# Kernel optimization log

Hardware: AMD Instinct MI355X
Metric: run time of the kernel (lower is better)

## Reference

```python
import jax, jax.numpy as jnp
import numpy as np

B, TQ, TK, D, R, H = 4, 2048, 2048, 1024, 64, 512
TAU_BASE, ASTRO_DECAY = 1.0, 0.95


def setup_inputs() -> dict:
    key = jax.random.key(0)
    ks = jax.random.split(key, 20)
    xav = lambda k, din, dout: jax.random.uniform(k, (din, dout), jnp.float32, -1.0, 1.0) * np.sqrt(6.0 / (din + dout))
    inp = {
        'q_in': jax.random.normal(ks[0], (B, TQ, D), jnp.float32),
        'k_in': jax.random.normal(ks[1], (B, TK, D), jnp.float32),
        'v_in': jax.random.normal(ks[2], (B, TK, D), jnp.float32),
        'astrocyte_state': jnp.zeros((B,), jnp.float32),
        'Wq': xav(ks[3], D, D), 'bq': jnp.zeros((D,), jnp.float32),
        'Wk': xav(ks[4], D, D), 'bk': jnp.zeros((D,), jnp.float32),
        'Wv': xav(ks[5], D, D), 'bv': jnp.zeros((D,), jnp.float32),
        'Wo': xav(ks[6], D, D), 'bo': jnp.zeros((D,), jnp.float32),
        # orthonormal role rows (R <= D): QR of a random D x R matrix, rows = Q^T
        'role_matrix': jnp.linalg.qr(jax.random.normal(ks[7], (D, R), jnp.float32))[0].T,
        'Wr1': xav(ks[8], D, H), 'br1': jnp.zeros((H,), jnp.float32),
        'Wr2': xav(ks[9], H, R),
        'astro_scale': jnp.ones((1,), jnp.float32),
    }
    return inp


def _l2norm(x, axis=-1, eps=1e-12):
    return x / jnp.clip(jnp.linalg.norm(x, axis=axis, keepdims=True), eps)


def _bind_vectors(a, b):
    # holographic (circular-convolution) binding via FFT along feature dim
    n = a.shape[-1]
    return jnp.fft.irfft(jnp.fft.rfft(a, axis=-1) * jnp.fft.rfft(b, axis=-1), n=n, axis=-1)


def _compute_surprise(Q):
    # per-token surprise: RMS-normalized L2 magnitude of projected queries -> (B, T_q)
    return jnp.linalg.norm(Q, axis=-1) / np.sqrt(Q.shape[-1])


def reference(q_in, k_in, v_in, astrocyte_state, Wq, bq, Wk, bk, Wv, bv, Wo, bo,
              role_matrix, Wr1, br1, Wr2, astro_scale):
    Q = q_in @ Wq + bq                      # (B,TQ,D)
    K = k_in @ Wk + bk                      # (B,TK,D)
    V = v_in @ Wv + bv                      # (B,TK,D)

    role_mat_norm = _l2norm(role_matrix)    # (R,D)
    role_logits = jax.nn.relu(K @ Wr1 + br1) @ Wr2          # (B,TK,R)
    role_weights = jax.nn.softmax(role_logits, axis=-1)
    role_vecs = role_weights @ role_mat_norm                 # (B,TK,D)
    K_bound = _bind_vectors(K, role_vecs)                    # (B,TK,D)

    surprise = _compute_surprise(Q)                          # (B,TQ)
    mean_surprise = surprise.mean(axis=-1)                   # (B,)
    new_state = ASTRO_DECAY * astrocyte_state + (1.0 - ASTRO_DECAY) * mean_surprise
    tau_eff = TAU_BASE * jnp.clip(1.0 + astro_scale * new_state, 0.001)[:, None, None]

    q_n = _l2norm(Q)
    k_n = _l2norm(K_bound)
    cos_sim = jnp.einsum('bqd,bkd->bqk', q_n, k_n)           # (B,TQ,TK)
    x = (cos_sim + 1.0) * 0.5
    scores = jnp.clip(1.0 - tau_eff * (1.0 - x) ** 2, 0.0)   # Epanechnikov kernel
    attn = scores / jnp.clip(scores.sum(axis=-1, keepdims=True), 1e-9)
    context = jnp.einsum('bqk,bkd->bqd', attn, V)
    output = context @ Wo + bo
    return output, new_state
```

## Files before the change

kernel.cpp:

```cpp
#include <hip/hip_runtime.h>
#include <stdint.h>


#define Bq 4
#define Tq 2048
#define Dd 1024
#define NT 8192
#define Hh 512
#define Rr_ 64
#define FP 640
#define F2 1280

typedef unsigned short ushort_t;
typedef short s16x8 __attribute__((ext_vector_type(8)));
typedef float floatx4 __attribute__((ext_vector_type(4)));

__device__ __forceinline__ float b2f(ushort_t s) {
  unsigned u = (unsigned)s << 16;
  return __builtin_bit_cast(float, u);
}
__device__ __forceinline__ ushort_t f2b(float f) {
  unsigned u = __builtin_bit_cast(unsigned, f);
  unsigned r = (u + 0x7fffu + ((u >> 16) & 1u)) >> 16;
  return (ushort_t)r;
}

__device__ __forceinline__ void load_lds16(const void* g, void* l) {
  __builtin_amdgcn_global_load_lds((__attribute__((address_space(1))) void*)(g),
                                   (__attribute__((address_space(3))) void*)(l),
                                   16, 0, 0);
}

__global__ __launch_bounds__(256) void gemm_bt(
    const ushort_t* __restrict__ A, const ushort_t* __restrict__ Bt,
    float* __restrict__ C, ushort_t* __restrict__ Cbf,
    const float* __restrict__ bias, const float* __restrict__ tau,
    float* __restrict__ rowsum, int rsStride, int rsMode,
    int K, int lda, int ldb, int ldc,
    long long sA, long long sB, long long sC, int flags)
{
  __shared__ __align__(16) ushort_t As[128 * 32];
  __shared__ __align__(16) ushort_t Bs[128 * 32];

  const int bz   = blockIdx.z;
  const ushort_t* Ab = A + (size_t)bz * sA;
  const ushort_t* Bb = Bt + (size_t)bz * sB;
  const int tm   = blockIdx.y * 128;
  const int tn   = blockIdx.x * 128;
  const int tid  = threadIdx.x;
  const int wave = tid >> 6;
  const int lane = tid & 63;
  const int wm   = (wave & 1) << 6;
  const int wn   = (wave >> 1) << 6;
  const int sr   = lane >> 2;
  const int sc   = (lane & 3) << 3;
  const int fr   = lane & 15;
  const int fk   = (lane >> 4) << 3;

  floatx4 acc[4][4] = {};

  for (int k0 = 0; k0 < K; k0 += 32) {
    {
      const ushort_t* gA0 = Ab + (size_t)(tm + wave * 16 + sr) * lda + (k0 + sc);
      const ushort_t* gA1 = gA0 + (size_t)64 * lda;
      char* lA = (char*)As + wave * 1024;
      load_lds16(gA0, lA);
      load_lds16(gA1, lA + 4096);
      const ushort_t* gB0 = Bb + (size_t)(tn + wave * 16 + sr) * ldb + (k0 + sc);
      const ushort_t* gB1 = gB0 + (size_t)64 * ldb;
      char* lB = (char*)Bs + wave * 1024;
      load_lds16(gB0, lB);
      load_lds16(gB1, lB + 4096);
    }
    __syncthreads();
    s16x8 af[4], bfv[4];
#pragma unroll
    for (int i = 0; i < 4; i++)
      af[i] = *(const s16x8*)&As[(wm + i * 16 + fr) * 32 + fk];
#pragma unroll
    for (int j = 0; j < 4; j++)
      bfv[j] = *(const s16x8*)&Bs[(wn + j * 16 + fr) * 32 + fk];
#pragma unroll
    for (int i = 0; i < 4; i++)
#pragma unroll
      for (int j = 0; j < 4; j++)
        acc[i][j] = __builtin_amdgcn_mfma_f32_16x16x32_bf16(af[i], bfv[j], acc[i][j], 0, 0, 0);
    __syncthreads();
  }

  const float tv = tau ? tau[bz] : 0.f;
  float*   Cp  = C   ? C   + (size_t)bz * sC : nullptr;
  ushort_t* Cb = Cbf ? Cbf + (size_t)bz * sC : nullptr;
#pragma unroll
  for (int i = 0; i < 4; i++) {
#pragma unroll
    for (int r = 0; r < 4; r++) {
      const int row = tm + wm + i * 16 + (lane >> 4) * 4 + r;
      float rsum = 0.f;
      float dinv = 1.f;
      if (rsMode == 3)
        dinv = 1.f / fmaxf(rowsum[(size_t)bz * rsStride + row], 1e-9f);
#pragma unroll
      for (int j = 0; j < 4; j++) {
        const int col = tn + wn + j * 16 + (lane & 15);
        float v = acc[i][j][r];
        if (bias) v += bias[col];
        if (flags & 1) v = fmaxf(v, 0.f);
        if (tau) { float d = 1.0f - v; v = fmaxf(1.0f - tv * 0.25f * d * d, 0.f); }
        if (rsMode == 3) v *= dinv;
        rsum += (rsMode == 2) ? v * v : v;
        if (Cp) Cp[(size_t)row * ldc + col] = v;
        if (Cb) Cb[(size_t)row * ldc + col] = f2b(v);
      }
      if (rsMode == 1 || rsMode == 2) {
        rsum += __shfl_xor(rsum, 1);
        rsum += __shfl_xor(rsum, 2);
        rsum += __shfl_xor(rsum, 4);
        rsum += __shfl_xor(rsum, 8);
        if ((lane & 15) == 0)
          atomicAdd(&rowsum[(size_t)bz * rsStride + row], rsum);
      }
    }
  }
}

__global__ __launch_bounds__(256) void castbf(const float* __restrict__ in,
                                              ushort_t* __restrict__ out, int n4) {
  int i = blockIdx.x * 256 + threadIdx.x;
  if (i >= n4) return;
  float4 v = ((const float4*)in)[i];
  ushort4 o;
  o.x = f2b(v.x); o.y = f2b(v.y); o.z = f2b(v.z); o.w = f2b(v.w);
  ((ushort4*)out)[i] = o;
}

__global__ __launch_bounds__(256) void tcast(const float* __restrict__ in,
                                             ushort_t* __restrict__ out,
                                             int RrN, int Cc, int Cp) {
  __shared__ float t[32][33];
  int r0 = blockIdx.x * 32, c0 = blockIdx.y * 32;
  int x = threadIdx.x, y = threadIdx.y;
  for (int dy = 0; dy < 32; dy += 8) {
    int r = r0 + y + dy, c = c0 + x;
    t[y + dy][x] = (c < Cc) ? in[(size_t)r * Cc + c] : 0.f;
  }
  __syncthreads();
  for (int dy = 0; dy < 32; dy += 8) {
    int c = c0 + y + dy, r = r0 + x;
    if (c < Cp) out[(size_t)c * RrN + r] = f2b(t[x][y + dy]);
  }
}

__global__ __launch_bounds__(512) void transpose_bf(const ushort_t* __restrict__ in,
                                                    ushort_t* __restrict__ out,
                                                    int RrN, int Cc, long long sIn, long long sOut) {
  __shared__ ushort_t t[64][65];
  int z = blockIdx.z;
  int r0 = blockIdx.y * 64, c0 = blockIdx.x * 64;
  int x = threadIdx.x, y = threadIdx.y;
  const ushort_t* ip = in + (size_t)z * sIn;
  ushort_t* op = out + (size_t)z * sOut;
  for (int dy = 0; dy < 64; dy += 8)
    t[y + dy][x] = ip[(size_t)(r0 + y + dy) * Cc + c0 + x];
  __syncthreads();
  for (int dy = 0; dy < 64; dy += 8)
    op[(size_t)(c0 + y + dy) * RrN + r0 + x] = t[x][y + dy];
}

__global__ __launch_bounds__(256) void rolenorm(const float* __restrict__ rm,
                                                ushort_t* __restrict__ rmn) {
  int r = blockIdx.x, tid = threadIdx.x;
  float4 v = ((const float4*)(rm + (size_t)r * 1024))[tid];
  float s = v.x * v.x + v.y * v.y + v.z * v.z + v.w * v.w;
#pragma unroll
  for (int m = 1; m < 64; m <<= 1) s += __shfl_xor(s, m);
  __shared__ float red[6];
  if ((tid & 63) == 0) red[tid >> 6] = s;
  __syncthreads();
  if (tid == 0) red[4] = 1.f / fmaxf(sqrtf(red[0] + red[1] + red[2] + red[3]), 1e-12f);
  __syncthreads();
  float inv = red[4];
  ushort4 o;
  o.x = f2b(v.x * inv); o.y = f2b(v.y * inv); o.z = f2b(v.z * inv); o.w = f2b(v.w * inv);
  ((ushort4*)(rmn + (size_t)r * 1024))[tid] = o;
}

__global__ __launch_bounds__(256) void rfn_kernel(const ushort_t* __restrict__ rmn,
                                                  const ushort_t* __restrict__ ftab,
                                                  ushort_t* __restrict__ RFnT) {
  int f = blockIdx.x;
  int t = threadIdx.x;
  int r = t >> 2, part = t & 3;
  const ushort_t* fr = ftab + (size_t)f * 1024 + part * 256;
  const ushort_t* rr = rmn + (size_t)r * 1024 + part * 256;
  float s = 0.f;
#pragma unroll 4
  for (int i = 0; i < 32; i++) {
    s16x8 a = *(const s16x8*)(fr + i * 8);
    s16x8 b = *(const s16x8*)(rr + i * 8);
#pragma unroll
    for (int j = 0; j < 8; j++) s += b2f((ushort_t)a[j]) * b2f((ushort_t)b[j]);
  }
  s += __shfl_xor(s, 1);
  s += __shfl_xor(s, 2);
  if (part == 0) RFnT[(size_t)f * 128 + r] = f2b(s);
}

__global__ __launch_bounds__(256) void scale_rows(const ushort_t* __restrict__ in,
                                                  ushort_t* __restrict__ out,
                                                  const float* __restrict__ sumsq) {
  int gid = blockIdx.x * 256 + threadIdx.x;
  int row = gid >> 7;
  int c0 = (gid & 127) << 3;
  float inv = 1.f / fmaxf(sqrtf(sumsq[row]), 1e-12f);
  const s16x8* p = (const s16x8*)(in + (size_t)row * 1024 + c0);
  s16x8 v = *p;
  s16x8 o;
#pragma unroll
  for (int i = 0; i < 8; i++) o[i] = (short)f2b(b2f((ushort_t)v[i]) * inv);
  *(s16x8*)(out + (size_t)row * 1024 + c0) = o;
}

__global__ __launch_bounds__(256) void surprise_sum(const float* __restrict__ sumsq,
                                                    float* __restrict__ ssum) {
  int row = blockIdx.x * 256 + threadIdx.x;
  float nrm = sqrtf(sumsq[row]);
#pragma unroll
  for (int m = 1; m < 64; m <<= 1) nrm += __shfl_xor(nrm, m);
  if ((threadIdx.x & 63) == 0) atomicAdd(&ssum[row >> 11], nrm);
}

__global__ void finalize_astro(const float* __restrict__ ssum, const float* __restrict__ astro,
                               const float* __restrict__ ascale, float* __restrict__ tau,
                               float* __restrict__ outTail) {
  int b = threadIdx.x;
  if (b < Bq) {
    float mean = ssum[b] * (1.f / (32.f * 2048.f));
    float ns = 0.95f * astro[b] + 0.05f * mean;
    tau[b] = fmaxf(1.f + ascale[0] * ns, 0.001f);
    outTail[b] = ns;
  }
}

__global__ __launch_bounds__(256) void softmax64(const float* __restrict__ logits,
                                                 ushort_t* __restrict__ out) {
  int row = blockIdx.x * 4 + (threadIdx.x >> 6);
  int lane = threadIdx.x & 63;
  float x = logits[(size_t)row * 128 + lane];
  float m = x;
#pragma unroll
  for (int s = 1; s < 64; s <<= 1) m = fmaxf(m, __shfl_xor(m, s));
  float e = expf(x - m);
  float sum = e;
#pragma unroll
  for (int s = 1; s < 64; s <<= 1) sum += __shfl_xor(sum, s);
  out[(size_t)row * 64 + lane] = f2b(e / sum);
}

__global__ __launch_bounds__(256) void gen_ftab(ushort_t* __restrict__ ftab) {
  const float TW = 6.283185307179586f / 1024.f;
  int idx = blockIdx.x * 256 + threadIdx.x;
  int rowf = idx >> 10, k = idx & 1023;
  int f = rowf < FP ? rowf : rowf - FP;
  float v = 0.f;
  if (f <= 512) {
    float th = (float)((f * k) & 1023) * TW;
    float sv, cv; sincosf(th, &sv, &cv);
    v = (rowf < FP) ? cv : -sv;
  }
  ftab[idx] = f2b(v);
}
__global__ __launch_bounds__(256) void gen_itab(ushort_t* __restrict__ itab) {
  const float TW = 6.283185307179586f / 1024.f;
  int idx = blockIdx.x * 256 + threadIdx.x;
  int n = idx / F2;
  int c = idx - n * F2;
  int f = c < FP ? c : c - FP;
  float v = 0.f;
  if (f <= 512) {
    float w = (f == 0 || f == 512) ? (1.f / 1024.f) : (2.f / 1024.f);
    float th = (float)((f * n) & 1023) * TW;
    float sv, cv; sincosf(th, &sv, &cv);
    v = (c < FP) ? w * cv : -w * sv;
  }
  itab[idx] = f2b(v);
}

__global__ __launch_bounds__(256) void fftmul(const ushort_t* __restrict__ KF,
                                              const ushort_t* __restrict__ RF,
                                              ushort_t* __restrict__ P) {
  int idx = blockIdx.x * 256 + threadIdx.x;
  int t = idx / FP;
  int f = idx - t * FP;
  size_t base = (size_t)t * F2;
  float a = b2f(KF[base + f]), b = b2f(KF[base + FP + f]);
  float c = b2f(RF[base + f]), d = b2f(RF[base + FP + f]);
  P[base + f]      = f2b(a * c - b * d);
  P[base + FP + f] = f2b(a * d + b * c);
}

static constexpr size_t OFF_RS    = 0;
static constexpr size_t OFF_SSQQ  = 32768;
static constexpr size_t OFF_SSQK  = 65536;
static constexpr size_t OFF_SSUM  = 98304;
static constexpr size_t OFF_TAU   = 98320;
static constexpr size_t OFF_WQT   = 98816;
static constexpr size_t OFF_WKT   = OFF_WQT  + 2097152;
static constexpr size_t OFF_WVT   = OFF_WKT  + 2097152;
static constexpr size_t OFF_WOT   = OFF_WVT  + 2097152;
static constexpr size_t OFF_WR1T  = OFF_WOT  + 2097152;
static constexpr size_t OFF_WR2T  = OFF_WR1T + 1048576;
static constexpr size_t OFF_RMN   = OFF_WR2T + 131072;
static constexpr size_t OFF_FTAB  = OFF_RMN  + 131072;
static constexpr size_t OFF_ITAB  = OFF_FTAB + 2621440;
static constexpr size_t OFF_RFNT  = OFF_ITAB + 2621440;
static constexpr size_t OFF_R1    = OFF_RFNT + 327680;
static constexpr size_t OFF_R2    = OFF_R1   + 20971520;
static constexpr size_t OFF_R3    = OFF_R2   + 20971520;
static constexpr size_t OFF_R4    = OFF_R3   + 20971520;
static constexpr size_t OFF_R5    = OFF_R4   + 16777216;
static constexpr size_t OFF_R6    = OFF_R5   + 16777216;
static constexpr size_t OFF_R7    = OFF_R6   + 16777216;
static constexpr size_t OFF_R8    = OFF_R7   + 16777216;
static constexpr size_t OFF_HID   = OFF_R8   + 16777216;
static constexpr size_t OFF_LOGI  = OFF_HID  + 8388608;
static constexpr size_t OFF_RW    = OFF_LOGI + 4194304;
static constexpr size_t OFF_SB    = OFF_RW   + 1048576;
static constexpr size_t WS_NEEDED = OFF_SB   + 33554432;

static inline void launch_gemm(hipStream_t s, const ushort_t* A, const ushort_t* Bt,
                               float* C, ushort_t* Cbf, const float* bias, const float* tau,
                               float* rowsum, int rsStride, int rsMode,
                               int M, int N, int K, int lda, int ldb, int ldc,
                               long long sA, long long sB, long long sC, int Z, int flags) {
  dim3 g(N / 128, M / 128, Z), b(256);
  gemm_bt<<<g, b, 0, s>>>(A, Bt, C, Cbf, bias, tau, rowsum, rsStride, rsMode,
                          K, lda, ldb, ldc, sA, sB, sC, flags);
}

extern "C" void kernel_launch(void* const* d_in, const int* in_sizes, int n_in,
                              void* d_out, int out_size, void* d_ws, size_t ws_size,
                              hipStream_t stream) {
  (void)in_sizes; (void)n_in; (void)out_size;
  if (ws_size < WS_NEEDED) return;

  const float* q_in  = (const float*)d_in[0];
  const float* k_in  = (const float*)d_in[1];
  const float* v_in  = (const float*)d_in[2];
  const float* astro = (const float*)d_in[3];
  const float* Wq    = (const float*)d_in[4];
  const float* bq    = (const float*)d_in[5];
  const float* Wk    = (const float*)d_in[6];
  const float* bk    = (const float*)d_in[7];
  const float* Wv    = (const float*)d_in[8];
  const float* bv    = (const float*)d_in[9];
  const float* Wo    = (const float*)d_in[10];
  const float* bo    = (const float*)d_in[11];
  const float* roleM = (const float*)d_in[12];
  const float* Wr1   = (const float*)d_in[13];
  const float* br1   = (const float*)d_in[14];
  const float* Wr2   = (const float*)d_in[15];
  const float* ascl  = (const float*)d_in[16];

  char* ws = (char*)d_ws;
  float*    rowsumS = (float*)(ws + OFF_RS);
  float*    ssqQ    = (float*)(ws + OFF_SSQQ);
  float*    ssqK    = (float*)(ws + OFF_SSQK);
  float*    ssum    = (float*)(ws + OFF_SSUM);
  float*    tau     = (float*)(ws + OFF_TAU);
  ushort_t* WqT  = (ushort_t*)(ws + OFF_WQT);
  ushort_t* WkT  = (ushort_t*)(ws + OFF_WKT);
  ushort_t* WvT  = (ushort_t*)(ws + OFF_WVT);
  ushort_t* WoT  = (ushort_t*)(ws + OFF_WOT);
  ushort_t* Wr1T = (ushort_t*)(ws + OFF_WR1T);
  ushort_t* Wr2T = (ushort_t*)(ws + OFF_WR2T);
  ushort_t* rmn  = (ushort_t*)(ws + OFF_RMN);
  ushort_t* FTab = (ushort_t*)(ws + OFF_FTAB);
  ushort_t* ITab = (ushort_t*)(ws + OFF_ITAB);
  ushort_t* RFnT = (ushort_t*)(ws + OFF_RFNT);
  ushort_t* qbf  = (ushort_t*)(ws + OFF_R1);
  ushort_t* KF   = (ushort_t*)(ws + OFF_R1);
  ushort_t* kinb = (ushort_t*)(ws + OFF_R2);
  ushort_t* RF   = (ushort_t*)(ws + OFF_R2);
  ushort_t* vinb = (ushort_t*)(ws + OFF_R3);
  ushort_t* Pb   = (ushort_t*)(ws + OFF_R3);
  ushort_t* qraw = (ushort_t*)(ws + OFF_R4);
  ushort_t* kn   = (ushort_t*)(ws + OFF_R4);
  ushort_t* qn   = (ushort_t*)(ws + OFF_R5);
  ushort_t* kp   = (ushort_t*)(ws + OFF_R6);
  ushort_t* ctx  = (ushort_t*)(ws + OFF_R6);
  ushort_t* vp   = (ushort_t*)(ws + OFF_R7);
  ushort_t* kbraw= (ushort_t*)(ws + OFF_R7);
  ushort_t* vT   = (ushort_t*)(ws + OFF_R8);
  ushort_t* hid  = (ushort_t*)(ws + OFF_HID);
  float*    logi = (float*)(ws + OFF_LOGI);
  ushort_t* rw   = (ushort_t*)(ws + OFF_RW);
  ushort_t* Sb   = (ushort_t*)(ws + OFF_SB);
  float*    out  = (float*)d_out;

  hipMemsetAsync(ws, 0, 98320, stream);

  tcast<<<dim3(32, 32), dim3(32, 8), 0, stream>>>(Wq, WqT, 1024, 1024, 1024);
  tcast<<<dim3(32, 32), dim3(32, 8), 0, stream>>>(Wk, WkT, 1024, 1024, 1024);
  tcast<<<dim3(32, 32), dim3(32, 8), 0, stream>>>(Wv, WvT, 1024, 1024, 1024);
  tcast<<<dim3(32, 32), dim3(32, 8), 0, stream>>>(Wo, WoT, 1024, 1024, 1024);
  tcast<<<dim3(32, 16), dim3(32, 8), 0, stream>>>(Wr1, Wr1T, 1024, 512, 512);
  tcast<<<dim3(16, 4),  dim3(32, 8), 0, stream>>>(Wr2, Wr2T, 512, 64, 128);
  rolenorm<<<64, 256, 0, stream>>>(roleM, rmn);
  gen_ftab<<<(F2 * 1024) / 256, 256, 0, stream>>>(FTab);
  gen_itab<<<(1024 * F2) / 256, 256, 0, stream>>>(ITab);
  rfn_kernel<<<F2, 256, 0, stream>>>(rmn, FTab, RFnT);

  castbf<<<8192, 256, 0, stream>>>(q_in, qbf, NT * Dd / 4);
  launch_gemm(stream, qbf, WqT, nullptr, qraw, bq, nullptr, ssqQ, 0, 2,
              NT, Dd, Dd, Dd, Dd, Dd, 0, 0, 0, 1, 0);
  scale_rows<<<NT / 2, 256, 0, stream>>>(qraw, qn, ssqQ);
  surprise_sum<<<NT / 256, 256, 0, stream>>>(ssqQ, ssum);
  finalize_astro<<<1, 64, 0, stream>>>(ssum, astro, ascl, tau, out + (size_t)NT * Dd);

  castbf<<<8192, 256, 0, stream>>>(k_in, kinb, NT * Dd / 4);
  launch_gemm(stream, kinb, WkT, nullptr, kp, bk, nullptr, nullptr, 0, 0,
              NT, Dd, Dd, Dd, Dd, Dd, 0, 0, 0, 1, 0);

  castbf<<<8192, 256, 0, stream>>>(v_in, vinb, NT * Dd / 4);
  launch_gemm(stream, vinb, WvT, nullptr, vp, bv, nullptr, nullptr, 0, 0,
              NT, Dd, Dd, Dd, Dd, Dd, 0, 0, 0, 1, 0);
  transpose_bf<<<dim3(16, 32, Bq), dim3(64, 8), 0, stream>>>(
      vp, vT, Tq, Dd, (long long)Tq * Dd, (long long)Dd * Tq);

  launch_gemm(stream, kp, Wr1T, nullptr, hid, br1, nullptr, nullptr, 0, 0,
              NT, Hh, Dd, Dd, Dd, Hh, 0, 0, 0, 1, 1 );
  launch_gemm(stream, hid, Wr2T, logi, nullptr, nullptr, nullptr, nullptr, 0, 0,
              NT, 128, Hh, Hh, Hh, 128, 0, 0, 0, 1, 0);
  softmax64<<<NT / 4, 256, 0, stream>>>(logi, rw);

  launch_gemm(stream, kp, FTab, nullptr, KF, nullptr, nullptr, nullptr, 0, 0,
              NT, F2, Dd, Dd, Dd, F2, 0, 0, 0, 1, 0);
  launch_gemm(stream, rw, RFnT, nullptr, RF, nullptr, nullptr, nullptr, 0, 0,
              NT, F2, Rr_, Rr_, 128, F2, 0, 0, 0, 1, 0);
  fftmul<<<(NT * FP) / 256, 256, 0, stream>>>(KF, RF, Pb);
  launch_gemm(stream, Pb, ITab, nullptr, kbraw, nullptr, nullptr, ssqK, 0, 2,
              NT, Dd, F2, F2, F2, Dd, 0, 0, 0, 1, 0);
  scale_rows<<<NT / 2, 256, 0, stream>>>(kbraw, kn, ssqK);

  launch_gemm(stream, qn, kn, nullptr, Sb, nullptr, tau, rowsumS, Tq, 1,
              Tq, Tq, Dd, Dd, Dd, Tq,
              (long long)Tq * Dd, (long long)Tq * Dd, (long long)Tq * Tq, Bq, 0);
  launch_gemm(stream, Sb, vT, nullptr, ctx, nullptr, nullptr, rowsumS, Tq, 3,
              Tq, Dd, Tq, Tq, Tq, Dd,
              (long long)Tq * Tq, (long long)Dd * Tq, (long long)Tq * Dd, Bq, 0);

  launch_gemm(stream, ctx, WoT, out, nullptr, bo, nullptr, nullptr, 0, 0,
              NT, Dd, Dd, Dd, Dd, Dd, 0, 0, 0, 1, 0);
}
```

Before: 774.1 us.

## Fold normalizations into GEMM epilogues, compute V transposed, shrink DFT tables, swizzle LDS

Removes the scale_rows passes by applying per-row and per-column inverse norms as multipliers in the GEMM epilogue. The V projection is computed directly in transposed form, which drops the separate transpose kernel. The real DFT tables are packed from 1280 to 1024 columns, so the DFT GEMMs do less work. It also adds an XOR-style swizzle to the LDS load and read offsets to reduce bank conflicts, and merges the four weight cast-transposes into one launch. The risks are extra epilogue loads per element and a possible mismatch between the swizzle and the global_load_lds write layout.

```diff
diff --git a/kernel.cpp b/kernel.cpp
--- a/kernel.cpp
+++ b/kernel.cpp
@@ -8,8 +8,7 @@
 #define NT 8192
 #define Hh 512
 #define Rr_ 64
-#define FP 640
-#define F2 1280
+#define FQ 1024
 
 typedef unsigned short ushort_t;
 typedef short s16x8 __attribute__((ext_vector_type(8)));
@@ -34,7 +33,10 @@
 __global__ __launch_bounds__(256) void gemm_bt(
     const ushort_t* __restrict__ A, const ushort_t* __restrict__ Bt,
     float* __restrict__ C, ushort_t* __restrict__ Cbf,
-    const float* __restrict__ bias, const float* __restrict__ tau,
+    const float* __restrict__ bias_col, const float* __restrict__ bias_row,
+    const float* __restrict__ rmul, int rmulStride,
+    const float* __restrict__ cmul, int cmulStride,
+    const float* __restrict__ tau,
     float* __restrict__ rowsum, int rsStride, int rsMode,
     int K, int lda, int ldb, int ldc,
     long long sA, long long sB, long long sC, int flags)
@@ -53,9 +55,10 @@
   const int wm   = (wave & 1) << 6;
   const int wn   = (wave >> 1) << 6;
   const int sr   = lane >> 2;
-  const int sc   = (lane & 3) << 3;
+  const int cp   = lane & 3;
+  const int sc   = (((cp - (sr >> 1)) & 3) << 3);
   const int fr   = lane & 15;
-  const int fk   = (lane >> 4) << 3;
+  const int fk   = ((((lane >> 4) + (fr >> 1)) & 3) << 3);
 
   floatx4 acc[4][4] = {};
 
@@ -91,23 +94,28 @@
   const float tv = tau ? tau[bz] : 0.f;
   float*   Cp  = C   ? C   + (size_t)bz * sC : nullptr;
   ushort_t* Cb = Cbf ? Cbf + (size_t)bz * sC : nullptr;
+  float bcv[4], cmv[4];
+#pragma unroll
+  for (int j = 0; j < 4; j++) {
+    const int col = tn + wn + j * 16 + (lane & 15);
+    bcv[j] = bias_col ? bias_col[col] : 0.f;
+    cmv[j] = cmul ? cmul[(size_t)bz * cmulStride + col] : 1.f;
+  }
 #pragma unroll
   for (int i = 0; i < 4; i++) {
 #pragma unroll
     for (int r = 0; r < 4; r++) {
       const int row = tm + wm + i * 16 + (lane >> 4) * 4 + r;
+      const float rm = rmul ? rmul[(size_t)bz * rmulStride + row] : 1.f;
+      const float br = bias_row ? bias_row[row] : 0.f;
       float rsum = 0.f;
-      float dinv = 1.f;
-      if (rsMode == 3)
-        dinv = 1.f / fmaxf(rowsum[(size_t)bz * rsStride + row], 1e-9f);
 #pragma unroll
       for (int j = 0; j < 4; j++) {
         const int col = tn + wn + j * 16 + (lane & 15);
-        float v = acc[i][j][r];
-        if (bias) v += bias[col];
+        float v = acc[i][j][r] + bcv[j] + br;
+        v *= rm * cmv[j];
         if (flags & 1) v = fmaxf(v, 0.f);
         if (tau) { float d = 1.0f - v; v = fmaxf(1.0f - tv * 0.25f * d * d, 0.f); }
-        if (rsMode == 3) v *= dinv;
         rsum += (rsMode == 2) ? v * v : v;
         if (Cp) Cp[(size_t)row * ldc + col] = v;
         if (Cb) Cb[(size_t)row * ldc + col] = f2b(v);
@@ -134,6 +142,21 @@
   ((ushort4*)out)[i] = o;
 }
 
+struct TC4 { const float* in[4]; ushort_t* out[4]; };
+__global__ __launch_bounds__(256) void tcast4(TC4 p) {
+  __shared__ float t[32][33];
+  int z = blockIdx.z;
+  const float* in = p.in[z];
+  ushort_t* out = p.out[z];
+  int r0 = blockIdx.x * 32, c0 = blockIdx.y * 32;
+  int x = threadIdx.x, y = threadIdx.y;
+  for (int dy = 0; dy < 32; dy += 8)
+    t[y + dy][x] = in[(size_t)(r0 + y + dy) * 1024 + c0 + x];
+  __syncthreads();
+  for (int dy = 0; dy < 32; dy += 8)
+    out[(size_t)(c0 + y + dy) * 1024 + r0 + x] = f2b(t[x][y + dy]);
+}
+
 __global__ __launch_bounds__(256) void tcast(const float* __restrict__ in,
                                              ushort_t* __restrict__ out,
                                              int RrN, int Cc, int Cp) {
@@ -149,22 +172,6 @@
     int c = c0 + y + dy, r = r0 + x;
     if (c < Cp) out[(size_t)c * RrN + r] = f2b(t[x][y + dy]);
   }
-}
-
-__global__ __launch_bounds__(512) void transpose_bf(const ushort_t* __restrict__ in,
-                                                    ushort_t* __restrict__ out,
-                                                    int RrN, int Cc, long long sIn, long long sOut) {
-  __shared__ ushort_t t[64][65];
-  int z = blockIdx.z;
-  int r0 = blockIdx.y * 64, c0 = blockIdx.x * 64;
-  int x = threadIdx.x, y = threadIdx.y;
-  const ushort_t* ip = in + (size_t)z * sIn;
-  ushort_t* op = out + (size_t)z * sOut;
-  for (int dy = 0; dy < 64; dy += 8)
-    t[y + dy][x] = ip[(size_t)(r0 + y + dy) * Cc + c0 + x];
-  __syncthreads();
-  for (int dy = 0; dy < 64; dy += 8)
-    op[(size_t)(c0 + y + dy) * RrN + r0 + x] = t[x][y + dy];
 }
 
 __global__ __launch_bounds__(256) void rolenorm(const float* __restrict__ rm,
@@ -206,28 +213,28 @@
   if (part == 0) RFnT[(size_t)f * 128 + r] = f2b(s);
 }
 
-__global__ __launch_bounds__(256) void scale_rows(const ushort_t* __restrict__ in,
-                                                  ushort_t* __restrict__ out,
-                                                  const float* __restrict__ sumsq) {
-  int gid = blockIdx.x * 256 + threadIdx.x;
-  int row = gid >> 7;
-  int c0 = (gid & 127) << 3;
-  float inv = 1.f / fmaxf(sqrtf(sumsq[row]), 1e-12f);
-  const s16x8* p = (const s16x8*)(in + (size_t)row * 1024 + c0);
-  s16x8 v = *p;
-  s16x8 o;
-#pragma unroll
-  for (int i = 0; i < 8; i++) o[i] = (short)f2b(b2f((ushort_t)v[i]) * inv);
-  *(s16x8*)(out + (size_t)row * 1024 + c0) = o;
-}
-
-__global__ __launch_bounds__(256) void surprise_sum(const float* __restrict__ sumsq,
-                                                    float* __restrict__ ssum) {
+__global__ __launch_bounds__(256) void invnorm_surprise(const float* __restrict__ ssq,
+                                                        float* __restrict__ invn,
+                                                        float* __restrict__ ssum) {
   int row = blockIdx.x * 256 + threadIdx.x;
-  float nrm = sqrtf(sumsq[row]);
-#pragma unroll
-  for (int m = 1; m < 64; m <<= 1) nrm += __shfl_xor(nrm, m);
-  if ((threadIdx.x & 63) == 0) atomicAdd(&ssum[row >> 11], nrm);
+  float nrm = sqrtf(ssq[row]);
+  invn[row] = 1.f / fmaxf(nrm, 1e-12f);
+  float t = nrm;
+#pragma unroll
+  for (int m = 1; m < 64; m <<= 1) t += __shfl_xor(t, m);
+  if ((threadIdx.x & 63) == 0) atomicAdd(&ssum[row >> 11], t);
+}
+
+__global__ __launch_bounds__(256) void invnorm(const float* __restrict__ ssq,
+                                               float* __restrict__ invn) {
+  int row = blockIdx.x * 256 + threadIdx.x;
+  invn[row] = 1.f / fmaxf(sqrtf(ssq[row]), 1e-12f);
+}
+
+__global__ __launch_bounds__(256) void invrowsum(const float* __restrict__ rs,
+                                                 float* __restrict__ inv) {
+  int row = blockIdx.x * 256 + threadIdx.x;
+  inv[row] = 1.f / fmaxf(rs[row], 1e-9f);
 }
 
 __global__ void finalize_astro(const float* __restrict__ ssum, const float* __restrict__ astro,
@@ -260,28 +267,27 @@
 __global__ __launch_bounds__(256) void gen_ftab(ushort_t* __restrict__ ftab) {
   const float TW = 6.283185307179586f / 1024.f;
   int idx = blockIdx.x * 256 + threadIdx.x;
-  int rowf = idx >> 10, k = idx & 1023;
-  int f = rowf < FP ? rowf : rowf - FP;
-  float v = 0.f;
-  if (f <= 512) {
-    float th = (float)((f * k) & 1023) * TW;
-    float sv, cv; sincosf(th, &sv, &cv);
-    v = (rowf < FP) ? cv : -sv;
-  }
-  ftab[idx] = f2b(v);
+  int j = idx >> 10, k = idx & 1023;
+  int f = j <= 512 ? j : j - 512;
+  float th = (float)((f * k) & 1023) * TW;
+  float sv, cv; sincosf(th, &sv, &cv);
+  ftab[idx] = f2b(j <= 512 ? cv : -sv);
 }
 __global__ __launch_bounds__(256) void gen_itab(ushort_t* __restrict__ itab) {
   const float TW = 6.283185307179586f / 1024.f;
   int idx = blockIdx.x * 256 + threadIdx.x;
-  int n = idx / F2;
-  int c = idx - n * F2;
-  int f = c < FP ? c : c - FP;
-  float v = 0.f;
-  if (f <= 512) {
-    float w = (f == 0 || f == 512) ? (1.f / 1024.f) : (2.f / 1024.f);
+  int n = idx >> 10, j = idx & 1023;
+  float v;
+  if (j <= 512) {
+    float w = (j == 0 || j == 512) ? (1.f / 1024.f) : (2.f / 1024.f);
+    float th = (float)((j * n) & 1023) * TW;
+    float sv, cv; sincosf(th, &sv, &cv);
+    v = w * cv;
+  } else {
+    int f = j - 512;
     float th = (float)((f * n) & 1023) * TW;
     float sv, cv; sincosf(th, &sv, &cv);
-    v = (c < FP) ? w * cv : -w * sv;
+    v = -(2.f / 1024.f) * sv;
   }
   itab[idx] = f2b(v);
 }
@@ -290,21 +296,29 @@
                                               const ushort_t* __restrict__ RF,
                                               ushort_t* __restrict__ P) {
   int idx = blockIdx.x * 256 + threadIdx.x;
-  int t = idx / FP;
-  int f = idx - t * FP;
-  size_t base = (size_t)t * F2;
-  float a = b2f(KF[base + f]), b = b2f(KF[base + FP + f]);
-  float c = b2f(RF[base + f]), d = b2f(RF[base + FP + f]);
-  P[base + f]      = f2b(a * c - b * d);
-  P[base + FP + f] = f2b(a * d + b * c);
+  int t = idx >> 9;
+  int j = idx & 511;
+  size_t base = (size_t)t * FQ;
+  if (j == 0) {
+    P[base]       = f2b(b2f(KF[base]) * b2f(RF[base]));
+    P[base + 512] = f2b(b2f(KF[base + 512]) * b2f(RF[base + 512]));
+  } else {
+    float a = b2f(KF[base + j]), b = b2f(KF[base + 512 + j]);
+    float c = b2f(RF[base + j]), d = b2f(RF[base + 512 + j]);
+    P[base + j]       = f2b(a * c - b * d);
+    P[base + 512 + j] = f2b(a * d + b * c);
+  }
 }
 
 static constexpr size_t OFF_RS    = 0;
 static constexpr size_t OFF_SSQQ  = 32768;
 static constexpr size_t OFF_SSQK  = 65536;
-static constexpr size_t OFF_SSUM  = 98304;
-static constexpr size_t OFF_TAU   = 98320;
-static constexpr size_t OFF_WQT   = 98816;
+static constexpr size_t OFF_INVQ  = 98304;
+static constexpr size_t OFF_INVK  = 131072;
+static constexpr size_t OFF_INVRS = 163840;
+static constexpr size_t OFF_SSUM  = 196608;
+static constexpr size_t OFF_TAU   = 196864;
+static constexpr size_t OFF_WQT   = 197120;
 static constexpr size_t OFF_WKT   = OFF_WQT  + 2097152;
 static constexpr size_t OFF_WVT   = OFF_WKT  + 2097152;
 static constexpr size_t OFF_WOT   = OFF_WVT  + 2097152;
@@ -312,29 +326,32 @@
 static constexpr size_t OFF_WR2T  = OFF_WR1T + 1048576;
 static constexpr size_t OFF_RMN   = OFF_WR2T + 131072;
 static constexpr size_t OFF_FTAB  = OFF_RMN  + 131072;
-static constexpr size_t OFF_ITAB  = OFF_FTAB + 2621440;
-static constexpr size_t OFF_RFNT  = OFF_ITAB + 2621440;
-static constexpr size_t OFF_R1    = OFF_RFNT + 327680;
-static constexpr size_t OFF_R2    = OFF_R1   + 20971520;
-static constexpr size_t OFF_R3    = OFF_R2   + 20971520;
-static constexpr size_t OFF_R4    = OFF_R3   + 20971520;
-static constexpr size_t OFF_R5    = OFF_R4   + 16777216;
-static constexpr size_t OFF_R6    = OFF_R5   + 16777216;
-static constexpr size_t OFF_R7    = OFF_R6   + 16777216;
-static constexpr size_t OFF_R8    = OFF_R7   + 16777216;
-static constexpr size_t OFF_HID   = OFF_R8   + 16777216;
+static constexpr size_t OFF_ITAB  = OFF_FTAB + 2097152;
+static constexpr size_t OFF_RFNT  = OFF_ITAB + 2097152;
+static constexpr size_t OFF_B1    = OFF_RFNT + 262144;
+static constexpr size_t OFF_B2    = OFF_B1   + 16777216;
+static constexpr size_t OFF_B3    = OFF_B2   + 16777216;
+static constexpr size_t OFF_B4    = OFF_B3   + 16777216;
+static constexpr size_t OFF_B5    = OFF_B4   + 16777216;
+static constexpr size_t OFF_B6    = OFF_B5   + 16777216;
+static constexpr size_t OFF_B7    = OFF_B6   + 16777216;
+static constexpr size_t OFF_HID   = OFF_B7   + 16777216;
 static constexpr size_t OFF_LOGI  = OFF_HID  + 8388608;
 static constexpr size_t OFF_RW    = OFF_LOGI + 4194304;
 static constexpr size_t OFF_SB    = OFF_RW   + 1048576;
 static constexpr size_t WS_NEEDED = OFF_SB   + 33554432;
 
 static inline void launch_gemm(hipStream_t s, const ushort_t* A, const ushort_t* Bt,
-                               float* C, ushort_t* Cbf, const float* bias, const float* tau,
-                               float* rowsum, int rsStride, int rsMode,
+                               float* Cf, ushort_t* Cb,
+                               const float* bias_col, const float* bias_row,
+                               const float* rmul, int rmulStride,
+                               const float* cmul, int cmulStride,
+                               const float* tau, float* rowsum, int rsStride, int rsMode,
                                int M, int N, int K, int lda, int ldb, int ldc,
                                long long sA, long long sB, long long sC, int Z, int flags) {
   dim3 g(N / 128, M / 128, Z), b(256);
-  gemm_bt<<<g, b, 0, s>>>(A, Bt, C, Cbf, bias, tau, rowsum, rsStride, rsMode,
+  gemm_bt<<<g, b, 0, s>>>(A, Bt, Cf, Cb, bias_col, bias_row, rmul, rmulStride,
+                          cmul, cmulStride, tau, rowsum, rsStride, rsMode,
                           K, lda, ldb, ldc, sA, sB, sC, flags);
 }
 
@@ -366,6 +383,9 @@
   float*    rowsumS = (float*)(ws + OFF_RS);
   float*    ssqQ    = (float*)(ws + OFF_SSQQ);
   float*    ssqK    = (float*)(ws + OFF_SSQK);
+  float*    invQ    = (float*)(ws + OFF_INVQ);
+  float*    invK    = (float*)(ws + OFF_INVK);
+  float*    invRS   = (float*)(ws + OFF_INVRS);
   float*    ssum    = (float*)(ws + OFF_SSUM);
   float*    tau     = (float*)(ws + OFF_TAU);
   ushort_t* WqT  = (ushort_t*)(ws + OFF_WQT);
@@ -378,78 +398,84 @@
   ushort_t* FTab = (ushort_t*)(ws + OFF_FTAB);
   ushort_t* ITab = (ushort_t*)(ws + OFF_ITAB);
   ushort_t* RFnT = (ushort_t*)(ws + OFF_RFNT);
-  ushort_t* qbf  = (ushort_t*)(ws + OFF_R1);
-  ushort_t* KF   = (ushort_t*)(ws + OFF_R1);
-  ushort_t* kinb = (ushort_t*)(ws + OFF_R2);
-  ushort_t* RF   = (ushort_t*)(ws + OFF_R2);
-  ushort_t* vinb = (ushort_t*)(ws + OFF_R3);
-  ushort_t* Pb   = (ushort_t*)(ws + OFF_R3);
-  ushort_t* qraw = (ushort_t*)(ws + OFF_R4);
-  ushort_t* kn   = (ushort_t*)(ws + OFF_R4);
-  ushort_t* qn   = (ushort_t*)(ws + OFF_R5);
-  ushort_t* kp   = (ushort_t*)(ws + OFF_R6);
-  ushort_t* ctx  = (ushort_t*)(ws + OFF_R6);
-  ushort_t* vp   = (ushort_t*)(ws + OFF_R7);
-  ushort_t* kbraw= (ushort_t*)(ws + OFF_R7);
-  ushort_t* vT   = (ushort_t*)(ws + OFF_R8);
+  ushort_t* qbf  = (ushort_t*)(ws + OFF_B1);
+  ushort_t* KF   = (ushort_t*)(ws + OFF_B1);
+  ushort_t* kinb = (ushort_t*)(ws + OFF_B2);
+  ushort_t* RF   = (ushort_t*)(ws + OFF_B2);
+  ushort_t* vinb = (ushort_t*)(ws + OFF_B3);
+  ushort_t* Pb   = (ushort_t*)(ws + OFF_B3);
+  ushort_t* qraw = (ushort_t*)(ws + OFF_B4);
+  ushort_t* kbraw= (ushort_t*)(ws + OFF_B5);
+  ushort_t* kp   = (ushort_t*)(ws + OFF_B6);
+  ushort_t* ctx  = (ushort_t*)(ws + OFF_B6);
+  ushort_t* vT   = (ushort_t*)(ws + OFF_B7);
   ushort_t* hid  = (ushort_t*)(ws + OFF_HID);
   float*    logi = (float*)(ws + OFF_LOGI);
   ushort_t* rw   = (ushort_t*)(ws + OFF_RW);
   ushort_t* Sb   = (ushort_t*)(ws + OFF_SB);
   float*    out  = (float*)d_out;
 
-  hipMemsetAsync(ws, 0, 98320, stream);
-
-  tcast<<<dim3(32, 32), dim3(32, 8), 0, stream>>>(Wq, WqT, 1024, 1024, 1024);
-  tcast<<<dim3(32, 32), dim3(32, 8), 0, stream>>>(Wk, WkT, 1024, 1024, 1024);
-  tcast<<<dim3(32, 32), dim3(32, 8), 0, stream>>>(Wv, WvT, 1024, 1024, 1024);
-  tcast<<<dim3(32, 32), dim3(32, 8), 0, stream>>>(Wo, WoT, 1024, 1024, 1024);
+  hipMemsetAsync(ws, 0, OFF_SSUM + 256, stream);
+
+  TC4 tc4;
+  tc4.in[0] = Wq; tc4.in[1] = Wk; tc4.in[2] = Wv; tc4.in[3] = Wo;
+  tc4.out[0] = WqT; tc4.out[1] = WkT; tc4.out[2] = WvT; tc4.out[3] = WoT;
+  tcast4<<<dim3(32, 32, 4), dim3(32, 8), 0, stream>>>(tc4);
   tcast<<<dim3(32, 16), dim3(32, 8), 0, stream>>>(Wr1, Wr1T, 1024, 512, 512);
   tcast<<<dim3(16, 4),  dim3(32, 8), 0, stream>>>(Wr2, Wr2T, 512, 64, 128);
   rolenorm<<<64, 256, 0, stream>>>(roleM, rmn);
-  gen_ftab<<<(F2 * 1024) / 256, 256, 0, stream>>>(FTab);
-  gen_itab<<<(1024 * F2) / 256, 256, 0, stream>>>(ITab);
-  rfn_kernel<<<F2, 256, 0, stream>>>(rmn, FTab, RFnT);
+  gen_ftab<<<(FQ * 1024) / 256, 256, 0, stream>>>(FTab);
+  gen_itab<<<(1024 * FQ) / 256, 256, 0, stream>>>(ITab);
+  rfn_kernel<<<FQ, 256, 0, stream>>>(rmn, FTab, RFnT);
 
   castbf<<<8192, 256, 0, stream>>>(q_in, qbf, NT * Dd / 4);
-  launch_gemm(stream, qbf, WqT, nullptr, qraw, bq, nullptr, ssqQ, 0, 2,
+  launch_gemm(stream, qbf, WqT, nullptr, qraw, bq, nullptr,
+              nullptr, 0, nullptr, 0, nullptr, ssqQ, 0, 2,
               NT, Dd, Dd, Dd, Dd, Dd, 0, 0, 0, 1, 0);
-  scale_rows<<<NT / 2, 256, 0, stream>>>(qraw, qn, ssqQ);
-  surprise_sum<<<NT / 256, 256, 0, stream>>>(ssqQ, ssum);
+  invnorm_surprise<<<NT / 256, 256, 0, stream>>>(ssqQ, invQ, ssum);
   finalize_astro<<<1, 64, 0, stream>>>(ssum, astro, ascl, tau, out + (size_t)NT * Dd);
 
   castbf<<<8192, 256, 0, stream>>>(k_in, kinb, NT * Dd / 4);
-  launch_gemm(stream, kinb, WkT, nullptr, kp, bk, nullptr, nullptr, 0, 0,
+  launch_gemm(stream, kinb, WkT, nullptr, kp, bk, nullptr,
+              nullptr, 0, nullptr, 0, nullptr, nullptr, 0, 0,
               NT, Dd, Dd, Dd, Dd, Dd, 0, 0, 0, 1, 0);
 
   castbf<<<8192, 256, 0, stream>>>(v_in, vinb, NT * Dd / 4);
-  launch_gemm(stream, vinb, WvT, nullptr, vp, bv, nullptr, nullptr, 0, 0,
-              NT, Dd, Dd, Dd, Dd, Dd, 0, 0, 0, 1, 0);
-  transpose_bf<<<dim3(16, 32, Bq), dim3(64, 8), 0, stream>>>(
-      vp, vT, Tq, Dd, (long long)Tq * Dd, (long long)Dd * Tq);
-
-  launch_gemm(stream, kp, Wr1T, nullptr, hid, br1, nullptr, nullptr, 0, 0,
+  launch_gemm(stream, WvT, vinb, nullptr, vT, nullptr, bv,
+              nullptr, 0, nullptr, 0, nullptr, nullptr, 0, 0,
+              Dd, NT, Dd, Dd, Dd, NT, 0, 0, 0, 1, 0);
+
+  launch_gemm(stream, kp, Wr1T, nullptr, hid, br1, nullptr,
+              nullptr, 0, nullptr, 0, nullptr, nullptr, 0, 0,
               NT, Hh, Dd, Dd, Dd, Hh, 0, 0, 0, 1, 1 );
-  launch_gemm(stream, hid, Wr2T, logi, nullptr, nullptr, nullptr, nullptr, 0, 0,
+  launch_gemm(stream, hid, Wr2T, logi, nullptr, nullptr, nullptr,
+              nullptr, 0, nullptr, 0, nullptr, nullptr, 0, 0,
               NT, 128, Hh, Hh, Hh, 128, 0, 0, 0, 1, 0);
   softmax64<<<NT / 4, 256, 0, stream>>>(logi, rw);
 
-  launch_gemm(stream, kp, FTab, nullptr, KF, nullptr, nullptr, nullptr, 0, 0,
-              NT, F2, Dd, Dd, Dd, F2, 0, 0, 0, 1, 0);
-  launch_gemm(stream, rw, RFnT, nullptr, RF, nullptr, nullptr, nullptr, 0, 0,
-              NT, F2, Rr_, Rr_, 128, F2, 0, 0, 0, 1, 0);
-  fftmul<<<(NT * FP) / 256, 256, 0, stream>>>(KF, RF, Pb);
-  launch_gemm(stream, Pb, ITab, nullptr, kbraw, nullptr, nullptr, ssqK, 0, 2,
-              NT, Dd, F2, F2, F2, Dd, 0, 0, 0, 1, 0);
-  scale_rows<<<NT / 2, 256, 0, stream>>>(kbraw, kn, ssqK);
-
-  launch_gemm(stream, qn, kn, nullptr, Sb, nullptr, tau, rowsumS, Tq, 1,
+  launch_gemm(stream, kp, FTab, nullptr, KF, nullptr, nullptr,
+              nullptr, 0, nullptr, 0, nullptr, nullptr, 0, 0,
+              NT, FQ, Dd, Dd, Dd, FQ, 0, 0, 0, 1, 0);
+  launch_gemm(stream, rw, RFnT, nullptr, RF, nullptr, nullptr,
+              nullptr, 0, nullptr, 0, nullptr, nullptr, 0, 0,
+              NT, FQ, Rr_, Rr_, 128, FQ, 0, 0, 0, 1, 0);
+  fftmul<<<(NT * 512) / 256, 256, 0, stream>>>(KF, RF, Pb);
+  launch_gemm(stream, Pb, ITab, nullptr, kbraw, nullptr, nullptr,
+              nullptr, 0, nullptr, 0, nullptr, ssqK, 0, 2,
+              NT, Dd, FQ, FQ, FQ, Dd, 0, 0, 0, 1, 0);
+  invnorm<<<NT / 256, 256, 0, stream>>>(ssqK, invK);
+
+  launch_gemm(stream, qraw, kbraw, nullptr, Sb, nullptr, nullptr,
+              invQ, Tq, invK, Tq, tau, rowsumS, Tq, 1,
               Tq, Tq, Dd, Dd, Dd, Tq,
               (long long)Tq * Dd, (long long)Tq * Dd, (long long)Tq * Tq, Bq, 0);
-  launch_gemm(stream, Sb, vT, nullptr, ctx, nullptr, nullptr, rowsumS, Tq, 3,
-              Tq, Dd, Tq, Tq, Tq, Dd,
-              (long long)Tq * Tq, (long long)Dd * Tq, (long long)Tq * Dd, Bq, 0);
-
-  launch_gemm(stream, ctx, WoT, out, nullptr, bo, nullptr, nullptr, 0, 0,
+  invrowsum<<<NT / 256, 256, 0, stream>>>(rowsumS, invRS);
+  launch_gemm(stream, Sb, vT, nullptr, ctx, nullptr, nullptr,
+              invRS, Tq, nullptr, 0, nullptr, nullptr, 0, 0,
+              Tq, Dd, Tq, Tq, NT, Dd,
+              (long long)Tq * Tq, (long long)Tq, (long long)Tq * Dd, Bq, 0);
+
+  launch_gemm(stream, ctx, WoT, out, nullptr, bo, nullptr,
+              nullptr, 0, nullptr, 0, nullptr, nullptr, 0, 0,
               NT, Dd, Dd, Dd, Dd, Dd, 0, 0, 0, 1, 0);
 }
```

Measured after the change: 677.0 us. -12.5%, faster.
